# Kernel tuning notes

Hardware: AMD Instinct MI355X
Metric: run time of the kernel (lower is better)

Reference implementation:

```python
import jax, jax.numpy as jnp
import numpy as np

HIDDEN = 768
NUM_HEADS = 12
HEAD_DIM = HIDDEN // NUM_HEADS


def setup_inputs() -> dict:
    key = jax.random.key(0)
    ks = jax.random.split(key, 10)
    B, S = 4, 2048
    scale = 1.0 / np.sqrt(HIDDEN)
    inp = {
        "hidden_states": jax.random.normal(ks[0], (B, S, HIDDEN), dtype=jnp.float32),
        "attention_mask": jnp.ones((B, S), dtype=jnp.float32),
        "Wq": jax.random.normal(ks[1], (HIDDEN, HIDDEN), dtype=jnp.float32) * scale,
        "bq": jnp.zeros((HIDDEN,), dtype=jnp.float32),
        "Wk": jax.random.normal(ks[2], (HIDDEN, HIDDEN), dtype=jnp.float32) * scale,
        "bk": jnp.zeros((HIDDEN,), dtype=jnp.float32),
        "Wv": jax.random.normal(ks[3], (HIDDEN, HIDDEN), dtype=jnp.float32) * scale,
        "bv": jnp.zeros((HIDDEN,), dtype=jnp.float32),
        "Wo": jax.random.normal(ks[4], (HIDDEN, HIDDEN), dtype=jnp.float32) * scale,
        "bo": jnp.zeros((HIDDEN,), dtype=jnp.float32),
    }
    return inp


def _split_heads(x):
    # [B,S,H] -> [B,nh,S,dh]
    B, S, _ = x.shape
    return x.reshape(B, S, NUM_HEADS, HEAD_DIM).transpose(0, 2, 1, 3)


def reference(hidden_states, attention_mask, Wq, bq, Wk, bk, Wv, bv, Wo, bo):
    # Linear projections (torch nn.Linear: x @ W.T + b; here W stored as [in,out])
    q = _split_heads(hidden_states @ Wq + bq)
    k = _split_heads(hidden_states @ Wk + bk)
    v = _split_heads(hidden_states @ Wv + bv)

    # scores: [B,nh,S,S]
    scores = jnp.einsum("bhqd,bhkd->bhqk", q, k) / np.sqrt(HEAD_DIM).astype(np.float32)

    # outer-product mask: [B,1,S,S], broadcast over heads
    ext = (attention_mask[:, :, None] * attention_mask[:, None, :])[:, None, :, :]
    scores = ext * scores - (1.0 - ext) * 1e9

    probs = jax.nn.softmax(scores, axis=-1)
    ctx = jnp.einsum("bhqk,bhkd->bhqd", probs, v)  # [B,nh,S,dh]
    B, _, S, _ = ctx.shape
    ctx = ctx.transpose(0, 2, 1, 3).reshape(B, S, HIDDEN)
    out = ctx @ Wo + bo
    # torch F.gelu default: exact (erf-based)
    return jax.nn.gelu(out, approximate=False)
```

## Files before the change

kernel.cpp:

```cpp
#include <hip/hip_runtime.h>
#include <math.h>

#define HIDDEN 768
#define NH 12
#define DH 64
#define SEQ 2048
#define BATCH 4

typedef __bf16 bf16;
typedef bf16 bf16x4 __attribute__((ext_vector_type(4)));
typedef bf16 bf16x8 __attribute__((ext_vector_type(8)));
typedef float f32x4 __attribute__((ext_vector_type(4)));

__device__ __forceinline__ void load_lds16(const void* g, void* l) {
    __builtin_amdgcn_global_load_lds(
        (__attribute__((address_space(1))) void*)g,
        (__attribute__((address_space(3))) void*)l, 16, 0, 0);
}

__global__ __launch_bounds__(256) void prep_xw(
    const float* __restrict__ X, bf16* __restrict__ Xb,
    const float* __restrict__ Wq, const float* __restrict__ Wk,
    const float* __restrict__ Wv, const float* __restrict__ Wo,
    bf16* __restrict__ Wt, bf16* __restrict__ Wot_hi,
    bf16* __restrict__ Wot_lo) {
    const int bid = blockIdx.x;
    const int tid = threadIdx.x;

    if (bid < 3072) {
        const size_t i = ((size_t)bid * 256 + tid) * 8;
        float4 a = *(const float4*)(X + i);
        float4 b = *(const float4*)(X + i + 4);
        bf16x8 o = {(bf16)a.x, (bf16)a.y, (bf16)a.z, (bf16)a.w,
                    (bf16)b.x, (bf16)b.y, (bf16)b.z, (bf16)b.w};
        *(bf16x8*)(Xb + i) = o;
        return;
    }

    __shared__ float Ts[64][68];
    const int r = bid - 3072;
    const int z = r / 144;
    const int rem = r - z * 144;
    const int n0 = (rem % 12) * 64, k0 = (rem / 12) * 64;
    const float* W = (z == 0) ? Wq : (z == 1) ? Wk : (z == 2) ? Wv : Wo;

    {
        const int rr = tid >> 2, c = (tid & 3) << 4;
        const float* src = W + (size_t)(k0 + rr) * HIDDEN + n0 + c;
#pragma unroll
        for (int j = 0; j < 4; ++j)
            *(float4*)&Ts[rr][c + 4 * j] = *(const float4*)(src + 4 * j);
    }
    __syncthreads();

    const int nl = tid >> 2, kc = (tid & 3) << 4;
    float v[16];
#pragma unroll
    for (int j = 0; j < 16; ++j) v[j] = Ts[kc + j][nl];

    if (z < 3) {
        bf16 hi[16];
#pragma unroll
        for (int j = 0; j < 16; ++j) hi[j] = (bf16)v[j];
        const size_t off = (size_t)(z * HIDDEN + n0 + nl) * HIDDEN + k0 + kc;
        *(bf16x8*)(Wt + off) = *(bf16x8*)&hi[0];
        *(bf16x8*)(Wt + off + 8) = *(bf16x8*)&hi[8];
    } else {
        bf16 hi[16], lo[16];
#pragma unroll
        for (int j = 0; j < 16; ++j) {
            hi[j] = (bf16)v[j];
            lo[j] = (bf16)(v[j] - (float)hi[j]);
        }
        const size_t off = (size_t)(n0 + nl) * HIDDEN + k0 + kc;
        *(bf16x8*)(Wot_hi + off) = *(bf16x8*)&hi[0];
        *(bf16x8*)(Wot_hi + off + 8) = *(bf16x8*)&hi[8];
        *(bf16x8*)(Wot_lo + off) = *(bf16x8*)&lo[0];
        *(bf16x8*)(Wot_lo + off + 8) = *(bf16x8*)&lo[8];
    }
}

__global__ __launch_bounds__(256, 3) void gemm_qkv(
    const bf16* __restrict__ Xb, const bf16* __restrict__ Wt,
    const float* __restrict__ bq, const float* __restrict__ bk,
    const float* __restrict__ bv, bf16* __restrict__ q_out,
    bf16* __restrict__ k_out, bf16* __restrict__ v_out) {
    __shared__ bf16 As[2][128 * 32];
    __shared__ bf16 Bs[2][192 * 32];

    const int tid = threadIdx.x;
    const int ln = tid & 63, wv = tid >> 6;
    const int quad = ln >> 4, l16 = ln & 15;
    const int wm = wv >> 1, wn = wv & 1;

    const int wg = blockIdx.x;
    const int xcd = wg & 7, i6 = wg >> 3;
    const int n0 = (i6 % 12) * 192;
    const int m0 = (xcd * 8 + i6 / 12) * 128;

    f32x4 acc[4][6];
#pragma unroll
    for (int i = 0; i < 4; ++i)
#pragma unroll
        for (int j = 0; j < 6; ++j) acc[i][j] = (f32x4){0.f, 0.f, 0.f, 0.f};

    const int srow = ln >> 2;
    const int bcol_sw = ((ln & 3) << 4) ^ (((ln >> 3) & 3) << 4);
    const char* gA =
        (const char*)Xb + ((size_t)(m0 + wv * 32 + srow) * HIDDEN) * 2 + bcol_sw;
    const char* gB =
        (const char*)Wt + ((size_t)(n0 + wv * 48 + srow) * HIDDEN) * 2 + bcol_sw;

    const int fsw = ((l16 >> 1) & 3) << 4;

    auto STAGE = [&](int b, int k0) {
#pragma unroll
        for (int j = 0; j < 2; ++j)
            load_lds16(gA + (size_t)k0 * 2 + (size_t)j * (16 * HIDDEN * 2),
                       &As[b][(wv * 32 + j * 16) * 32]);
#pragma unroll
        for (int j = 0; j < 3; ++j)
            load_lds16(gB + (size_t)k0 * 2 + (size_t)j * (16 * HIDDEN * 2),
                       &Bs[b][(wv * 48 + j * 16) * 32]);
    };

    auto COMPUTE = [&](int b) {
        bf16x8 ah[4], bh[6];
#pragma unroll
        for (int i = 0; i < 4; ++i)
            ah[i] = *(const bf16x8*)((const char*)&As[b][0] +
                                     (wm * 64 + i * 16 + l16) * 64 +
                                     ((quad * 16) ^ fsw));
#pragma unroll
        for (int i = 0; i < 6; ++i)
            bh[i] = *(const bf16x8*)((const char*)&Bs[b][0] +
                                     (wn * 96 + i * 16 + l16) * 64 +
                                     ((quad * 16) ^ fsw));
#pragma unroll
        for (int mi = 0; mi < 4; ++mi)
#pragma unroll
            for (int ni = 0; ni < 6; ++ni)
                acc[mi][ni] = __builtin_amdgcn_mfma_f32_16x16x32_bf16(
                    ah[mi], bh[ni], acc[mi][ni], 0, 0, 0);
    };

    STAGE(0, 0);
    __syncthreads();

    for (int step = 0; step < 24; step += 2) {
        if (step + 1 < 24) STAGE(1, (step + 1) * 32);
        COMPUTE(0);
        __syncthreads();
        if (step + 2 < 24) STAGE(0, (step + 2) * 32);
        COMPUTE(1);
        __syncthreads();
    }

    const int nb = n0 + wn * 96;
    const int which = nb / HIDDEN;
    const int nrel = nb - which * HIDDEN;

    if (which < 2) {
        const float scale = (which == 0) ? 0.18033688011112042f : 1.0f;
        const float* bias = (which == 0) ? bq : bk;
        bf16* dst = (which == 0) ? q_out : k_out;
#pragma unroll
        for (int ni = 0; ni < 6; ++ni) {
            const int nn = nrel + ni * 16;
            const int h = nn >> 6;
            const int dh = (nn & 63) + l16;
            const float bb = bias[nn + l16];
#pragma unroll
            for (int mi = 0; mi < 4; ++mi)
#pragma unroll
                for (int r = 0; r < 4; ++r) {
                    const int m = m0 + wm * 64 + mi * 16 + quad * 4 + r;
                    const int bi = m >> 11, s = m & (SEQ - 1);
                    dst[(((size_t)(bi * NH + h) * SEQ + s) << 6) + dh] =
                        (bf16)(scale * (acc[mi][ni][r] + bb));
                }
        }
    } else {
        const int bi = m0 >> 11;
        const int sbase = (m0 & (SEQ - 1)) + wm * 64;
#pragma unroll
        for (int ni = 0; ni < 6; ++ni) {
            const int nn = nrel + ni * 16;
            const int h = nn >> 6;
            const int dh = (nn & 63) + l16;
            const float bb = bv[nn + l16];
            bf16* vrow = v_out + ((size_t)(bi * NH + h) * DH + dh) * SEQ;
#pragma unroll
            for (int mi = 0; mi < 4; ++mi) {
                bf16x4 pk = {(bf16)(acc[mi][ni][0] + bb),
                             (bf16)(acc[mi][ni][1] + bb),
                             (bf16)(acc[mi][ni][2] + bb),
                             (bf16)(acc[mi][ni][3] + bb)};
                *(bf16x4*)(vrow + sbase + mi * 16 + quad * 4) = pk;
            }
        }
    }
}

__global__ __launch_bounds__(256) void attn_mfma(const bf16* __restrict__ Q,
                                                 const bf16* __restrict__ K,
                                                 const bf16* __restrict__ Vt,
                                                 const float* __restrict__ mask,
                                                 bf16* __restrict__ ctx_hi,
                                                 bf16* __restrict__ ctx_lo) {
    __shared__ bf16 Ks[64 * 64];
    __shared__ bf16 Vts[64 * 64];
    __shared__ bf16 Ps[128 * 64];
    __shared__ float Ms[SEQ];
    __shared__ int allones_s;

    const int tid = threadIdx.x;
    const int ln = tid & 63, w = tid >> 6;
    const int quad = ln >> 4, l16 = ln & 15;

    const int wg = blockIdx.x;
    const int logical = (wg & 7) * 96 + (wg >> 3);
    const int qt = logical & 15;
    const int h = (logical >> 4) % NH;
    const int b = logical / (16 * NH);

    const size_t bh = (size_t)b * NH + h;
    const bf16* Qp = Q + ((bh * SEQ + (size_t)qt * 128) << 6);
    const bf16* Kp = K + (bh * SEQ << 6);
    const bf16* Vp = Vt + (bh * DH) * SEQ;

    if (tid == 0) allones_s = 1;
    {
        float4 m0 = *(const float4*)(mask + (size_t)b * SEQ + tid * 8);
        float4 m1 = *(const float4*)(mask + (size_t)b * SEQ + tid * 8 + 4);
        *(float4*)&Ms[tid * 8] = m0;
        *(float4*)&Ms[tid * 8 + 4] = m1;
        bool ok = (m0.x == 1.f) & (m0.y == 1.f) & (m0.z == 1.f) &
                  (m0.w == 1.f) & (m1.x == 1.f) & (m1.y == 1.f) &
                  (m1.z == 1.f) & (m1.w == 1.f);
        __syncthreads();
        if (!ok) allones_s = 0;
    }
    __syncthreads();
    const bool fastmask = (allones_s != 0);

    bf16x8 qb[2][2];
#pragma unroll
    for (int qg = 0; qg < 2; ++qg)
#pragma unroll
        for (int hf = 0; hf < 2; ++hf)
            qb[qg][hf] = *(const bf16x8*)(Qp + ((w * 32 + qg * 16 + l16) << 6) +
                                          hf * 32 + quad * 8);
    float mq[2];
#pragma unroll
    for (int qg = 0; qg < 2; ++qg)
        mq[qg] = Ms[qt * 128 + w * 32 + qg * 16 + l16];

    float l_i[2] = {0.f, 0.f};
    f32x4 acc[4][2];
#pragma unroll
    for (int fd = 0; fd < 4; ++fd)
#pragma unroll
        for (int qg = 0; qg < 2; ++qg) acc[fd][qg] = (f32x4){0.f, 0.f, 0.f, 0.f};

    const int sr = tid >> 2, sc = (tid & 3) << 4;
    const int ssw = (sr & 7) << 3;
    const int d0 = sc ^ ssw, d1 = (sc + 8) ^ ssw;
    const bf16* kbase = Kp + ((size_t)sr << 6) + sc;
    const bf16* vbase = Vp + (size_t)sr * SEQ + sc;

    bf16x8 kr0, kr1, vr0, vr1;
    kr0 = *(const bf16x8*)kbase;
    kr1 = *(const bf16x8*)(kbase + 8);
    vr0 = *(const bf16x8*)vbase;
    vr1 = *(const bf16x8*)(vbase + 8);

    for (int kt = 0; kt < SEQ / 64; ++kt) {
        __syncthreads();
        *(bf16x8*)&Ks[sr * 64 + d0] = kr0;
        *(bf16x8*)&Ks[sr * 64 + d1] = kr1;
        *(bf16x8*)&Vts[sr * 64 + d0] = vr0;
        *(bf16x8*)&Vts[sr * 64 + d1] = vr1;
        __syncthreads();
        if (kt + 1 < SEQ / 64) {
            kr0 = *(const bf16x8*)(kbase + ((size_t)(kt + 1) << 12));
            kr1 = *(const bf16x8*)(kbase + ((size_t)(kt + 1) << 12) + 8);
            vr0 = *(const bf16x8*)(vbase + (kt + 1) * 64);
            vr1 = *(const bf16x8*)(vbase + (kt + 1) * 64 + 8);
        }

        const int fsw = (l16 & 7) << 3;
        f32x4 st[4][2];
#pragma unroll
        for (int f = 0; f < 4; ++f) {
            const int krow = (f * 16 + l16) * 64;
            bf16x8 ka0 = *(bf16x8*)&Ks[krow + ((quad * 8) ^ fsw)];
            bf16x8 ka1 = *(bf16x8*)&Ks[krow + ((32 + quad * 8) ^ fsw)];
#pragma unroll
            for (int qg = 0; qg < 2; ++qg) {
                f32x4 c = {0.f, 0.f, 0.f, 0.f};
                c = __builtin_amdgcn_mfma_f32_16x16x32_bf16(ka0, qb[qg][0], c, 0, 0, 0);
                c = __builtin_amdgcn_mfma_f32_16x16x32_bf16(ka1, qb[qg][1], c, 0, 0, 0);
                st[f][qg] = c;
            }
        }

        if (!fastmask) {
#pragma unroll
            for (int f = 0; f < 4; ++f) {
                const float4 mk4 = *(const float4*)&Ms[kt * 64 + f * 16 + quad * 4];
                const float mkk[4] = {mk4.x, mk4.y, mk4.z, mk4.w};
#pragma unroll
                for (int qg = 0; qg < 2; ++qg)
#pragma unroll
                    for (int r = 0; r < 4; ++r) {
                        const float ext = mq[qg] * mkk[r];
                        st[f][qg][r] =
                            ext * st[f][qg][r] - (1.0f - ext) * 1.4426950e9f;
                    }
            }
        }

#pragma unroll
        for (int qg = 0; qg < 2; ++qg) {
            const int row = w * 32 + qg * 16 + l16;
            const int sw = (row & 7) << 3;
            bf16* prow = &Ps[row * 64];
#pragma unroll
            for (int f = 0; f < 4; ++f) {
                float p0 = __builtin_amdgcn_exp2f(st[f][qg][0]);
                float p1 = __builtin_amdgcn_exp2f(st[f][qg][1]);
                float p2 = __builtin_amdgcn_exp2f(st[f][qg][2]);
                float p3 = __builtin_amdgcn_exp2f(st[f][qg][3]);
                l_i[qg] += (p0 + p1) + (p2 + p3);
                bf16x4 pk = {(bf16)p0, (bf16)p1, (bf16)p2, (bf16)p3};
                *(bf16x4*)&prow[(f * 16 + quad * 4) ^ sw] = pk;
            }
        }

        bf16x8 pb[2][2];
#pragma unroll
        for (int qg = 0; qg < 2; ++qg) {
            const int row = w * 32 + qg * 16 + l16;
            const int sw = (row & 7) << 3;
#pragma unroll
            for (int hf = 0; hf < 2; ++hf)
                pb[qg][hf] =
                    *(bf16x8*)&Ps[row * 64 + ((hf * 32 + quad * 8) ^ sw)];
        }
#pragma unroll
        for (int fd = 0; fd < 4; ++fd) {
            const int vrow = (fd * 16 + l16) * 64;
            bf16x8 va0 = *(bf16x8*)&Vts[vrow + ((quad * 8) ^ fsw)];
            bf16x8 va1 = *(bf16x8*)&Vts[vrow + ((32 + quad * 8) ^ fsw)];
#pragma unroll
            for (int qg = 0; qg < 2; ++qg) {
                f32x4 c = acc[fd][qg];
                c = __builtin_amdgcn_mfma_f32_16x16x32_bf16(va0, pb[qg][0], c, 0, 0, 0);
                c = __builtin_amdgcn_mfma_f32_16x16x32_bf16(va1, pb[qg][1], c, 0, 0, 0);
                acc[fd][qg] = c;
            }
        }
    }

#pragma unroll
    for (int qg = 0; qg < 2; ++qg) {
        l_i[qg] += __shfl_xor(l_i[qg], 16);
        l_i[qg] += __shfl_xor(l_i[qg], 32);
    }

#pragma unroll
    for (int qg = 0; qg < 2; ++qg) {
        const float inv = 1.0f / l_i[qg];
        const size_t row = (size_t)b * SEQ + qt * 128 + w * 32 + qg * 16 + l16;
#pragma unroll
        for (int fd = 0; fd < 4; ++fd) {
            bf16 hi[4], lo[4];
#pragma unroll
            for (int r = 0; r < 4; ++r) {
                const float o = acc[fd][qg][r] * inv;
                hi[r] = (bf16)o;
                lo[r] = (bf16)(o - (float)hi[r]);
            }
            const size_t off = row * HIDDEN + h * 64 + fd * 16 + quad * 4;
            *(bf16x4*)(ctx_hi + off) = *(bf16x4*)&hi[0];
            *(bf16x4*)(ctx_lo + off) = *(bf16x4*)&lo[0];
        }
    }
}

__global__ __launch_bounds__(256) void gemm_out(const bf16* __restrict__ Ah,
                                                const bf16* __restrict__ Al,
                                                const bf16* __restrict__ Bhi,
                                                const bf16* __restrict__ Blo,
                                                const float* __restrict__ bo,
                                                float* __restrict__ fout) {
    __shared__ bf16 Ash[2][128 * 32];
    __shared__ bf16 Asl[2][128 * 32];
    __shared__ bf16 Bsh[2][64 * 32];
    __shared__ bf16 Bsl[2][64 * 32];

    const int tid = threadIdx.x;
    const int ln = tid & 63, wv = tid >> 6;
    const int quad = ln >> 4, l16 = ln & 15;
    const int wm = wv >> 1, wn = wv & 1;

    const int wg = blockIdx.x;
    const int xcd = wg & 7, i6 = wg >> 3;
    const int n0 = (i6 % 12) * 64;
    const int m0 = (xcd * 8 + i6 / 12) * 128;

    f32x4 acc[4][2];
#pragma unroll
    for (int i = 0; i < 4; ++i)
#pragma unroll
        for (int j = 0; j < 2; ++j) acc[i][j] = (f32x4){0.f, 0.f, 0.f, 0.f};

    const int srow = ln >> 2;
    const int bcol_sw = ((ln & 3) << 4) ^ (((ln >> 3) & 3) << 4);
    const char* gAh =
        (const char*)Ah + ((size_t)(m0 + wv * 32 + srow) * HIDDEN) * 2 + bcol_sw;
    const char* gAl =
        (const char*)Al + ((size_t)(m0 + wv * 32 + srow) * HIDDEN) * 2 + bcol_sw;
    const char* gBh =
        (const char*)Bhi + ((size_t)(n0 + wv * 16 + srow) * HIDDEN) * 2 + bcol_sw;
    const char* gBl =
        (const char*)Blo + ((size_t)(n0 + wv * 16 + srow) * HIDDEN) * 2 + bcol_sw;

    const int fsw = ((l16 >> 1) & 3) << 4;

    auto STAGE = [&](int b, int k0) {
#pragma unroll
        for (int j = 0; j < 2; ++j) {
            load_lds16(gAh + (size_t)k0 * 2 + (size_t)j * (16 * HIDDEN * 2),
                       &Ash[b][(wv * 32 + j * 16) * 32]);
            load_lds16(gAl + (size_t)k0 * 2 + (size_t)j * (16 * HIDDEN * 2),
                       &Asl[b][(wv * 32 + j * 16) * 32]);
        }
        load_lds16(gBh + (size_t)k0 * 2, &Bsh[b][(wv * 16) * 32]);
        load_lds16(gBl + (size_t)k0 * 2, &Bsl[b][(wv * 16) * 32]);
    };

    auto COMPUTE = [&](int b) {
        bf16x8 ah[4], al[4], bh[2], bl[2];
#pragma unroll
        for (int i = 0; i < 4; ++i) {
            const int row = (wm * 64 + i * 16 + l16) * 64;
            ah[i] = *(const bf16x8*)((const char*)&Ash[b][0] + row +
                                     ((quad * 16) ^ fsw));
            al[i] = *(const bf16x8*)((const char*)&Asl[b][0] + row +
                                     ((quad * 16) ^ fsw));
        }
#pragma unroll
        for (int i = 0; i < 2; ++i) {
            const int row = (wn * 32 + i * 16 + l16) * 64;
            bh[i] = *(const bf16x8*)((const char*)&Bsh[b][0] + row +
                                     ((quad * 16) ^ fsw));
            bl[i] = *(const bf16x8*)((const char*)&Bsl[b][0] + row +
                                     ((quad * 16) ^ fsw));
        }
#pragma unroll
        for (int mi = 0; mi < 4; ++mi)
#pragma unroll
            for (int ni = 0; ni < 2; ++ni) {
                f32x4 c = acc[mi][ni];
                c = __builtin_amdgcn_mfma_f32_16x16x32_bf16(ah[mi], bh[ni], c, 0, 0, 0);
                c = __builtin_amdgcn_mfma_f32_16x16x32_bf16(ah[mi], bl[ni], c, 0, 0, 0);
                c = __builtin_amdgcn_mfma_f32_16x16x32_bf16(al[mi], bh[ni], c, 0, 0, 0);
                acc[mi][ni] = c;
            }
    };

    STAGE(0, 0);
    __syncthreads();

    for (int step = 0; step < 24; step += 2) {
        if (step + 1 < 24) STAGE(1, (step + 1) * 32);
        COMPUTE(0);
        __syncthreads();
        if (step + 2 < 24) STAGE(0, (step + 2) * 32);
        COMPUTE(1);
        __syncthreads();
    }

#pragma unroll
    for (int ni = 0; ni < 2; ++ni) {
        const int n = n0 + wn * 32 + ni * 16 + l16;
        const float bb = bo[n];
#pragma unroll
        for (int mi = 0; mi < 4; ++mi)
#pragma unroll
            for (int r = 0; r < 4; ++r) {
                const int m = m0 + wm * 64 + mi * 16 + quad * 4 + r;
                float x = acc[mi][ni][r] + bb;
                x = 0.5f * x * (1.0f + erff(x * 0.70710678118654752440f));
                fout[(size_t)m * HIDDEN + n] = x;
            }
    }
}

extern "C" void kernel_launch(void* const* d_in, const int* in_sizes, int n_in,
                              void* d_out, int out_size, void* d_ws, size_t ws_size,
                              hipStream_t stream) {
    const float* X    = (const float*)d_in[0];
    const float* mask = (const float*)d_in[1];
    const float* Wq   = (const float*)d_in[2];
    const float* bq   = (const float*)d_in[3];
    const float* Wk   = (const float*)d_in[4];
    const float* bk   = (const float*)d_in[5];
    const float* Wv   = (const float*)d_in[6];
    const float* bv   = (const float*)d_in[7];
    const float* Wo   = (const float*)d_in[8];
    const float* bo   = (const float*)d_in[9];
    float* out = (float*)d_out;

    char* w = (char*)d_ws;
    const size_t NE = (size_t)BATCH * SEQ * HIDDEN;
    bf16* q_ws   = (bf16*)w;  w += NE * 2;
    bf16* k_ws   = (bf16*)w;  w += NE * 2;
    bf16* vt_ws  = (bf16*)w;  w += NE * 2;
    bf16* ctx_hi = (bf16*)w;  w += NE * 2;
    bf16* ctx_lo = (bf16*)w;  w += NE * 2;
    bf16* Xb     = (bf16*)w;  w += NE * 2;
    bf16* Wt     = (bf16*)w;  w += (size_t)3 * HIDDEN * HIDDEN * 2;
    bf16* Wot_hi = (bf16*)w;  w += (size_t)HIDDEN * HIDDEN * 2;
    bf16* Wot_lo = (bf16*)w;  w += (size_t)HIDDEN * HIDDEN * 2;

    prep_xw<<<3648, 256, 0, stream>>>(X, Xb, Wq, Wk, Wv, Wo, Wt, Wot_hi,
                                      Wot_lo);
    gemm_qkv<<<dim3(768), 256, 0, stream>>>(Xb, Wt, bq, bk, bv, q_ws, k_ws,
                                            vt_ws);
    attn_mfma<<<dim3(16 * NH * BATCH), 256, 0, stream>>>(
        q_ws, k_ws, vt_ws, mask, ctx_hi, ctx_lo);
    gemm_out<<<dim3(768), 256, 0, stream>>>(ctx_hi, ctx_lo, Wot_hi, Wot_lo,
                                            bo, out);
}
```

Baseline: 248.4 us.

## Double-buffer attention K/V tiles with direct global-to-LDS loads

Replaces register-staged K/V prefetch with global_load_lds transfers into two LDS buffers, so the next tile streams into shared memory while MFMAs run on the current one. The XOR swizzle moves to the global source address, and the two barriers per iteration become one at the end of the loop. The mask copy in shared memory is stored as bf16 to make room for the second buffer. This removes the VGPR round-trip and a barrier per tile, at the cost of more LDS and reliance on correct wait semantics for the async loads; non-binary mask values would also lose precision.

```diff
diff --git a/kernel.cpp b/kernel.cpp
--- a/kernel.cpp
+++ b/kernel.cpp
@@ -208,10 +208,10 @@
                                                  const float* __restrict__ mask,
                                                  bf16* __restrict__ ctx_hi,
                                                  bf16* __restrict__ ctx_lo) {
-    __shared__ bf16 Ks[64 * 64];
-    __shared__ bf16 Vts[64 * 64];
+    __shared__ bf16 Ks[2][64 * 64];
+    __shared__ bf16 Vts[2][64 * 64];
     __shared__ bf16 Ps[128 * 64];
-    __shared__ float Ms[SEQ];
+    __shared__ bf16 Msb[SEQ];
     __shared__ int allones_s;
 
     const int tid = threadIdx.x;
@@ -233,8 +233,9 @@
     {
         float4 m0 = *(const float4*)(mask + (size_t)b * SEQ + tid * 8);
         float4 m1 = *(const float4*)(mask + (size_t)b * SEQ + tid * 8 + 4);
-        *(float4*)&Ms[tid * 8] = m0;
-        *(float4*)&Ms[tid * 8 + 4] = m1;
+        bf16x8 mb = {(bf16)m0.x, (bf16)m0.y, (bf16)m0.z, (bf16)m0.w,
+                     (bf16)m1.x, (bf16)m1.y, (bf16)m1.z, (bf16)m1.w};
+        *(bf16x8*)&Msb[tid * 8] = mb;
         bool ok = (m0.x == 1.f) & (m0.y == 1.f) & (m0.z == 1.f) &
                   (m0.w == 1.f) & (m1.x == 1.f) & (m1.y == 1.f) &
                   (m1.z == 1.f) & (m1.w == 1.f);
@@ -254,7 +255,7 @@
     float mq[2];
 #pragma unroll
     for (int qg = 0; qg < 2; ++qg)
-        mq[qg] = Ms[qt * 128 + w * 32 + qg * 16 + l16];
+        mq[qg] = (float)Msb[qt * 128 + w * 32 + qg * 16 + l16];
 
     float l_i[2] = {0.f, 0.f};
     f32x4 acc[4][2];
@@ -263,39 +264,37 @@
 #pragma unroll
         for (int qg = 0; qg < 2; ++qg) acc[fd][qg] = (f32x4){0.f, 0.f, 0.f, 0.f};
 
-    const int sr = tid >> 2, sc = (tid & 3) << 4;
-    const int ssw = (sr & 7) << 3;
-    const int d0 = sc ^ ssw, d1 = (sc + 8) ^ ssw;
-    const bf16* kbase = Kp + ((size_t)sr << 6) + sc;
-    const bf16* vbase = Vp + (size_t)sr * SEQ + sc;
-
-    bf16x8 kr0, kr1, vr0, vr1;
-    kr0 = *(const bf16x8*)kbase;
-    kr1 = *(const bf16x8*)(kbase + 8);
-    vr0 = *(const bf16x8*)vbase;
-    vr1 = *(const bf16x8*)(vbase + 8);
+    const int r8 = ln >> 3;
+    const int scol = ((ln & 7) << 4) ^ (r8 << 4);
+    const char* gK = (const char*)Kp + (size_t)(w * 16 + r8) * 128 + scol;
+    const char* gV =
+        (const char*)Vp + (size_t)(w * 16 + r8) * (SEQ * 2) + scol;
+
+    auto STAGE = [&](int buf, int kt) {
+#pragma unroll
+        for (int j = 0; j < 2; ++j) {
+            load_lds16(gK + ((size_t)kt << 13) + j * 1024,
+                       &Ks[buf][(w * 16 + j * 8) * 64]);
+            load_lds16(gV + (size_t)kt * 128 + (size_t)j * (8 * SEQ * 2),
+                       &Vts[buf][(w * 16 + j * 8) * 64]);
+        }
+    };
+
+    const int fsw = (l16 & 7) << 3;
+
+    STAGE(0, 0);
+    __syncthreads();
 
     for (int kt = 0; kt < SEQ / 64; ++kt) {
-        __syncthreads();
-        *(bf16x8*)&Ks[sr * 64 + d0] = kr0;
-        *(bf16x8*)&Ks[sr * 64 + d1] = kr1;
-        *(bf16x8*)&Vts[sr * 64 + d0] = vr0;
-        *(bf16x8*)&Vts[sr * 64 + d1] = vr1;
-        __syncthreads();
-        if (kt + 1 < SEQ / 64) {
-            kr0 = *(const bf16x8*)(kbase + ((size_t)(kt + 1) << 12));
-            kr1 = *(const bf16x8*)(kbase + ((size_t)(kt + 1) << 12) + 8);
-            vr0 = *(const bf16x8*)(vbase + (kt + 1) * 64);
-            vr1 = *(const bf16x8*)(vbase + (kt + 1) * 64 + 8);
-        }
-
-        const int fsw = (l16 & 7) << 3;
+        const int cur = kt & 1;
+        if (kt + 1 < SEQ / 64) STAGE(cur ^ 1, kt + 1);
+
         f32x4 st[4][2];
 #pragma unroll
         for (int f = 0; f < 4; ++f) {
             const int krow = (f * 16 + l16) * 64;
-            bf16x8 ka0 = *(bf16x8*)&Ks[krow + ((quad * 8) ^ fsw)];
-            bf16x8 ka1 = *(bf16x8*)&Ks[krow + ((32 + quad * 8) ^ fsw)];
+            bf16x8 ka0 = *(bf16x8*)&Ks[cur][krow + ((quad * 8) ^ fsw)];
+            bf16x8 ka1 = *(bf16x8*)&Ks[cur][krow + ((32 + quad * 8) ^ fsw)];
 #pragma unroll
             for (int qg = 0; qg < 2; ++qg) {
                 f32x4 c = {0.f, 0.f, 0.f, 0.f};
@@ -308,8 +307,10 @@
         if (!fastmask) {
 #pragma unroll
             for (int f = 0; f < 4; ++f) {
-                const float4 mk4 = *(const float4*)&Ms[kt * 64 + f * 16 + quad * 4];
-                const float mkk[4] = {mk4.x, mk4.y, mk4.z, mk4.w};
+                const bf16x4 mk4 =
+                    *(const bf16x4*)&Msb[kt * 64 + f * 16 + quad * 4];
+                const float mkk[4] = {(float)mk4[0], (float)mk4[1],
+                                      (float)mk4[2], (float)mk4[3]};
 #pragma unroll
                 for (int qg = 0; qg < 2; ++qg)
 #pragma unroll
@@ -351,8 +352,8 @@
 #pragma unroll
         for (int fd = 0; fd < 4; ++fd) {
             const int vrow = (fd * 16 + l16) * 64;
-            bf16x8 va0 = *(bf16x8*)&Vts[vrow + ((quad * 8) ^ fsw)];
-            bf16x8 va1 = *(bf16x8*)&Vts[vrow + ((32 + quad * 8) ^ fsw)];
+            bf16x8 va0 = *(bf16x8*)&Vts[cur][vrow + ((quad * 8) ^ fsw)];
+            bf16x8 va1 = *(bf16x8*)&Vts[cur][vrow + ((32 + quad * 8) ^ fsw)];
 #pragma unroll
             for (int qg = 0; qg < 2; ++qg) {
                 f32x4 c = acc[fd][qg];
@@ -361,6 +362,8 @@
                 acc[fd][qg] = c;
             }
         }
+
+        __syncthreads();
     }
 
 #pragma unroll
```

Result: slower. 261.5 us (+5.3%).
